# Kernel tuning notes

Hardware: AMD Instinct MI355X
Metric: run time of the kernel (lower is better)

Reference implementation:

```python
import jax, jax.numpy as jnp
import numpy as np

NUM_HEADS = 6
V = 25          # num_points (joints)
F = 64          # num_frames
T = F * V       # 1600 tokens
DIM = 216
HD = DIM // NUM_HEADS
SCALE = HD ** -0.5
MAX_HOP = 16    # hop-distance table size (distances clipped to MAX_HOP-1)
LN_EPS = 1e-5


def _ntu_hop_dist():
    # NTU RGB+D 25-joint skeleton edges (1-indexed)
    edges = [(1, 2), (2, 21), (3, 21), (4, 3), (5, 21), (6, 5), (7, 6), (8, 7),
             (9, 21), (10, 9), (11, 10), (12, 11), (13, 1), (14, 13), (15, 14),
             (16, 15), (17, 1), (18, 17), (19, 18), (20, 19), (22, 23), (23, 8),
             (24, 25), (25, 12)]
    D = np.full((V, V), 99, dtype=np.int64)
    np.fill_diagonal(D, 0)
    for a, b in edges:
        D[a - 1, b - 1] = 1
        D[b - 1, a - 1] = 1
    for k in range(V):  # Floyd-Warshall on tiny 25-node graph
        D = np.minimum(D, D[:, k:k + 1] + D[k:k + 1, :])
    return np.clip(D, 0, MAX_HOP - 1).astype(np.int32)


def setup_inputs() -> dict:
    key = jax.random.key(0)
    ks = jax.random.split(key, 16)
    s = 0.02  # trunc_normal_(std=0.02) init scale
    rn = lambda k, shape: jax.random.normal(k, shape, jnp.float32) * s
    return {
        "x": jax.random.normal(ks[0], (8, T, DIM), jnp.float32),
        "qkv_w": rn(ks[1], (3 * DIM, DIM)),
        "proj_w": rn(ks[2], (DIM, DIM)),
        "proj_b": jnp.zeros((DIM,), jnp.float32),
        "norm_w": jnp.ones((DIM,), jnp.float32),
        "norm_b": jnp.zeros((DIM,), jnp.float32),
        "norm1_w": jnp.ones((DIM,), jnp.float32),
        "norm1_b": jnp.zeros((DIM,), jnp.float32),
        "fc1_w": rn(ks[3], (4 * DIM, DIM)),
        "fc1_b": jnp.zeros((4 * DIM,), jnp.float32),
        "fc2_w": rn(ks[4], (DIM, 4 * DIM)),
        "fc2_b": jnp.zeros((DIM,), jnp.float32),
        "t_w1": rn(ks[5], (DIM, 1)),
        "t_b1": jnp.zeros((DIM,), jnp.float32),
        "t_w2": rn(ks[6], (NUM_HEADS, DIM)),
        "t_b2": jnp.zeros((NUM_HEADS,), jnp.float32),
        "h_w1": rn(ks[7], (DIM, 1)),
        "h_b1": jnp.zeros((DIM,), jnp.float32),
        "h_w2": rn(ks[8], (NUM_HEADS, DIM)),
        "h_b2": jnp.zeros((NUM_HEADS,), jnp.float32),
        "hop_dist": jnp.asarray(_ntu_hop_dist()),
    }


def _ln(x, w, b):
    mu = x.mean(-1, keepdims=True)
    var = jnp.mean((x - mu) ** 2, axis=-1, keepdims=True)
    return (x - mu) * jax.lax.rsqrt(var + LN_EPS) * w + b


def reference(x, qkv_w, proj_w, proj_b, norm_w, norm_b, norm1_w, norm1_b,
              fc1_w, fc1_b, fc2_w, fc2_b, t_w1, t_b1, t_w2, t_b2,
              h_w1, h_b1, h_w2, h_b2, hop_dist):
    N = x.shape[0]
    h = _ln(x, norm_w, norm_b)
    qkv = (h @ qkv_w.T).reshape(N, T, 3, NUM_HEADS, HD).transpose(2, 0, 3, 1, 4)
    q, k, v = qkv[0], qkv[1], qkv[2]                       # (N,H,T,HD)
    attn = jnp.einsum('nhqc,nhkc->nhqk', q, k)             # (N,H,T,T)

    # temporal relative position bias (depends only on relative frame offset)
    coords = jnp.arange(-(F - 1), F, dtype=jnp.float32)[:, None]       # (2F-1,1)
    tbl_t = jax.nn.relu(coords @ t_w1.T + t_b1) @ t_w2.T + t_b2        # (2F-1,H)
    fidx = jnp.arange(F)
    rel = fidx[:, None] - fidx[None, :] + (F - 1)                      # (F,F)
    bias_t = tbl_t[rel].transpose(2, 0, 1)                             # (H,F,F)
    bias_t = jnp.repeat(jnp.repeat(bias_t, V, axis=1), V, axis=2)      # (H,T,T)

    # hop relative position bias (skeleton hop distance, same every frame pair)
    hvals = jnp.arange(MAX_HOP, dtype=jnp.float32)[:, None]            # (MAX_HOP,1)
    tbl_h = jax.nn.relu(hvals @ h_w1.T + h_b1) @ h_w2.T + h_b2         # (MAX_HOP,H)
    bias_h = tbl_h[hop_dist].transpose(2, 0, 1)                        # (H,V,V)
    bias_h = jnp.tile(bias_h, (1, F, F))                               # (H,T,T)

    attn = (attn + bias_h + bias_t) * SCALE  # scale AFTER bias, as in source
    attn = jax.nn.softmax(attn, axis=-1)
    o = jnp.einsum('nhqk,nhkc->nhqc', attn, v)
    o = o.transpose(0, 2, 1, 3).reshape(N, T, DIM)
    o = o @ proj_w.T + proj_b

    x1 = x + o  # skip_proj is Identity (dim_in == dim)
    h1 = _ln(x1, norm1_w, norm1_b)
    m = jax.nn.gelu(h1 @ fc1_w.T + fc1_b, approximate=False) @ fc2_w.T + fc2_b
    return x1 + m
```

## Files before the change

kernel.cpp:

```cpp
#include <hip/hip_runtime.h>
#include <hip/hip_bf16.h>


#define NHEAD  6
#define TLEN   1600
#define DIMC   216
#define HDIM   36
#define NBATCH 8
#define MROWS  12800
#define QK_SCALE (1.f/6.f)
#define C2EXP 0.24022650695910072f

typedef __attribute__((ext_vector_type(8))) short s16x8;
typedef __attribute__((ext_vector_type(4))) float f32x4;

#define MFMA16(a,b,c) __builtin_amdgcn_mfma_f32_16x16x32_bf16((a),(b),(c),0,0,0)

__device__ __forceinline__ float  bf2f(ushort u){ return __uint_as_float((uint)u << 16); }
__device__ __forceinline__ ushort f2bf(float f){
  uint u = __float_as_uint(f);
  u += 0x7FFFu + ((u >> 16) & 1u);
  return (ushort)(u >> 16);
}
__device__ __forceinline__ uint cvtpk_bf16(float lo, float hi){
  uint r;
  asm("v_cvt_pk_bf16_f32 %0, %1, %2" : "=v"(r) : "v"(lo), "v"(hi));
  return r;
}
__device__ __forceinline__ float fexp2(float x){
  float r;
  asm("v_exp_f32 %0, %1" : "=v"(r) : "v"(x));
  return r;
}
__device__ __forceinline__ float frcp(float x){
  float r;
  asm("v_rcp_f32 %0, %1" : "=v"(r) : "v"(x));
  return r;
}
__device__ __forceinline__ void glds16(const ushort* g, ushort* l){
  __builtin_amdgcn_global_load_lds(
      (const __attribute__((address_space(1))) void*)g,
      (__attribute__((address_space(3))) void*)l, 16, 0, 0);
}

__global__ __launch_bounds__(256) void bias_tables_kernel(
    const float* __restrict__ t_w1, const float* __restrict__ t_b1,
    const float* __restrict__ t_w2, const float* __restrict__ t_b2,
    const float* __restrict__ h_w1, const float* __restrict__ h_b1,
    const float* __restrict__ h_w2, const float* __restrict__ h_b2,
    const int*  __restrict__ hop,
    float* __restrict__ bias_t, float* __restrict__ bias_h)
{
  __shared__ float tblh[16][NHEAD];
  int tid = threadIdx.x;
  if (tid < 127) {
    float xi = (float)(tid - 63);
    float acc[NHEAD] = {0.f,0.f,0.f,0.f,0.f,0.f};
    for (int d = 0; d < DIMC; ++d) {
      float r = fmaxf(fmaf(xi, t_w1[d], t_b1[d]), 0.f);
      #pragma unroll
      for (int h = 0; h < NHEAD; ++h) acc[h] = fmaf(r, t_w2[h*DIMC + d], acc[h]);
    }
    #pragma unroll
    for (int h = 0; h < NHEAD; ++h)
      bias_t[h*127 + tid] = (acc[h] + t_b2[h]) * C2EXP;
  }
  if (tid >= 128 && tid < 144) {
    int i = tid - 128;
    float xi = (float)i;
    float acc[NHEAD] = {0.f,0.f,0.f,0.f,0.f,0.f};
    for (int d = 0; d < DIMC; ++d) {
      float r = fmaxf(fmaf(xi, h_w1[d], h_b1[d]), 0.f);
      #pragma unroll
      for (int h = 0; h < NHEAD; ++h) acc[h] = fmaf(r, h_w2[h*DIMC + d], acc[h]);
    }
    #pragma unroll
    for (int h = 0; h < NHEAD; ++h) tblh[i][h] = acc[h] + h_b2[h];
  }
  __syncthreads();
  for (int i = tid; i < NHEAD*625; i += 256) {
    int h = i / 625, e = i - h*625;
    bias_h[i] = tblh[hop[e]][h];
  }
}

#define CP_QKV 157696
#define CP_PROJ 215040
#define CP_FC1 415744
#define CP_TOT 636928
#define PC_TOT (CP_TOT + NBATCH*NHEAD*TLEN)

__global__ __launch_bounds__(256) void padconv_kernel(
    const float* __restrict__ qkvw, const float* __restrict__ projw,
    const float* __restrict__ fc1w, const float* __restrict__ fc2w,
    ushort* __restrict__ dq, ushort* __restrict__ dp,
    ushort* __restrict__ d1, ushort* __restrict__ d2,
    const float* __restrict__ bh_raw,
    ushort* __restrict__ qb, ushort* __restrict__ kb)
{
  int idx = blockIdx.x*256 + threadIdx.x;
  if (idx < CP_TOT) {
    if (idx < CP_QKV) {
      int n = idx / 224, k = idx - n*224;
      dq[idx] = f2bf((n < 648 && k < 216) ? qkvw[n*216 + k] : 0.f);
    } else if (idx < CP_PROJ) {
      int i = idx - CP_QKV;
      int n = i / 224, k = i - n*224;
      dp[i] = f2bf((n < 216 && k < 216) ? projw[n*216 + k] : 0.f);
    } else if (idx < CP_FC1) {
      int i = idx - CP_PROJ;
      int n = i / 224, k = i - n*224;
      d1[i] = f2bf((n < 864 && k < 216) ? fc1w[n*216 + k] : 0.f);
    } else {
      int i = idx - CP_FC1;
      int n = i / 864, k = i - n*864;
      d2[i] = f2bf((n < 216) ? fc2w[n*864 + k] : 0.f);
    }
    return;
  }
  int i = idx - CP_TOT;
  if (i >= NBATCH*NHEAD*TLEN) return;
  int nh = i / TLEN, t = i - nh*TLEN;
  int h = nh % NHEAD;
  int vk = t % 25;
  size_t row = ((size_t)nh*TLEN + t) << 6;
  ushort4 z = {0,0,0,0};
  #pragma unroll
  for (int j = 0; j < 7; ++j) *(ushort4*)(qb + row + 36 + j*4) = z;
  qb[row + 36 + vk] = 0x3F80;
  #pragma unroll
  for (int j = 0; j < 25; ++j)
    kb[row + 36 + j] = f2bf(bh_raw[h*625 + j*25 + vk]);
  kb[row + 61] = 0; kb[row + 62] = 0; kb[row + 63] = 0;
}

__global__ __launch_bounds__(256) void ln_kernel(
    const float* __restrict__ x, const float* __restrict__ w,
    const float* __restrict__ b, ushort* __restrict__ out)
{
  int lane = threadIdx.x & 63;
  int row  = blockIdx.x * 4 + (threadIdx.x >> 6);
  const float* xr = x + (size_t)row * DIMC;
  float v0 = xr[lane];
  float v1 = xr[lane + 64];
  float v2 = xr[lane + 128];
  float v3 = (lane < 24) ? xr[lane + 192] : 0.f;
  float s1 = v0 + v1 + v2 + v3;
  float s2 = v0*v0 + v1*v1 + v2*v2 + v3*v3;
  #pragma unroll
  for (int m = 32; m; m >>= 1) { s1 += __shfl_xor(s1, m); s2 += __shfl_xor(s2, m); }
  float mu  = s1 * (1.f/216.f);
  float var = fmaxf(s2 * (1.f/216.f) - mu*mu, 0.f);
  float rs  = rsqrtf(var + 1e-5f);
  ushort* orow = out + (size_t)row * 224;
  orow[lane]       = f2bf((v0-mu)*rs*w[lane]       + b[lane]);
  orow[lane+64]    = f2bf((v1-mu)*rs*w[lane+64]    + b[lane+64]);
  orow[lane+128]   = f2bf((v2-mu)*rs*w[lane+128]   + b[lane+128]);
  if (lane < 32) {
    float vv = (lane < 24) ? (v3-mu)*rs*w[lane+192] + b[lane+192] : 0.f;
    orow[lane+192] = f2bf(vv);
  }
}

enum { EPI_QKV = 0, EPI_PROJ = 1, EPI_FC1 = 2, EPI_FC2 = 3 };

template<int EPI, int WM>
__global__ __launch_bounds__(256) void gemm_mfma(
    const ushort* __restrict__ A, const ushort* __restrict__ B,
    const float* __restrict__ bias, const float* __restrict__ res,
    float* __restrict__ outf, ushort* __restrict__ oq,
    ushort* __restrict__ ok, ushort* __restrict__ ov,
    int N, int K)
{
  constexpr int BM = WM*4;
  constexpr int NMF = WM/16;
  constexpr int APASS = (BM*4)/256;
  __shared__ ushort As[2][BM*32];
  __shared__ ushort Bs[2][64*32];

  int tid = threadIdx.x;
  int w = tid >> 6, lane = tid & 63, l15 = lane & 15, g = lane >> 4;
  int row0 = blockIdx.x*BM, col0 = blockIdx.y*64;
  const int NT = K >> 5;

  f32x4 acc[NMF][4];
  #pragma unroll
  for (int i = 0; i < NMF; ++i)
    #pragma unroll
    for (int nf = 0; nf < 4; ++nf) acc[i][nf] = (f32x4){0.f,0.f,0.f,0.f};

  #define STAGE(buf, t)                                                       \
  {                                                                           \
    int k0 = (t) << 5;                                                        \
    _Pragma("unroll")                                                         \
    for (int p = 0; p < APASS; ++p) {                                         \
      int idx = p*256 + tid;                                                  \
      int mf = idx >> 6, kq = (idx >> 4) & 3, r = idx & 15;                   \
      glds16(A + (size_t)(row0 + mf*16 + r)*K + k0 + kq*8,                    \
             &As[buf][(p*256 + w*64)*8]);                                     \
    }                                                                         \
    {                                                                         \
      int kq = (tid >> 4) & 3, r = tid & 15;                                  \
      glds16(B + (size_t)(col0 + w*16 + r)*K + k0 + kq*8,                     \
             &Bs[buf][w*512]);                                                \
    }                                                                         \
  }

  STAGE(0, 0)
  __syncthreads();

  for (int t = 0; t < NT; ++t) {
    int buf = t & 1;
    if (t + 1 < NT) STAGE(buf ^ 1, t + 1)
    #pragma unroll
    for (int i = 0; i < NMF; ++i) {
      s16x8 a = *(const s16x8*)&As[buf][((w*NMF + i)*64 + g*16 + l15)*8];
      #pragma unroll
      for (int nf = 0; nf < 4; ++nf) {
        s16x8 b = *(const s16x8*)&Bs[buf][(nf*64 + g*16 + l15)*8];
        acc[i][nf] = MFMA16(a, b, acc[i][nf]);
      }
    }
    __syncthreads();
  }
  #undef STAGE

  #pragma unroll
  for (int i = 0; i < NMF; ++i) {
    #pragma unroll
    for (int nf = 0; nf < 4; ++nf) {
      int c = col0 + nf*16 + l15;
      if (c >= N) continue;
      #pragma unroll
      for (int r = 0; r < 4; ++r) {
        int rr = row0 + w*WM + i*16 + 4*g + r;
        float v = acc[i][nf][r];
        if constexpr (EPI == EPI_QKV) {
          int s = c / DIMC, rem = c - s*DIMC;
          int hh = rem / HDIM, d = rem - hh*HDIM;
          int n = rr / TLEN, t = rr - n*TLEN;
          int nh = n*NHEAD + hh;
          ushort bv = f2bf(v);
          if (s == 0)      oq[(((size_t)nh*TLEN + t) << 6) + d] = bv;
          else if (s == 1) ok[(((size_t)nh*TLEN + t) << 6) + d] = bv;
          else {
            int tile = t >> 6, pos = t & 63;
            int ks2 = pos >> 5, kg = (pos >> 2) & 7, r2 = pos & 3;
            int sg = ((kg & 3) << 1) + (kg >> 2);
            int posp = ks2*32 + sg*4 + r2;
            int grs = (posp >> 3) ^ (d & 7);
            ov[((size_t)nh*HDIM + d)*TLEN + tile*64 + grs*8 + (posp & 7)] = bv;
          }
        } else if constexpr (EPI == EPI_PROJ) {
          outf[(size_t)rr*DIMC + c] = v + bias[c] + res[(size_t)rr*DIMC + c];
        } else if constexpr (EPI == EPI_FC1) {
          v += bias[c];
          float y = 0.7978845608f*(v + 0.044715f*v*v*v);
          float e = fexp2(-2.885390082f*y);
          v = v * frcp(1.f + e);
          oq[(size_t)rr*864 + c] = f2bf(v);
        } else {
          outf[(size_t)rr*DIMC + c] = v + bias[c] + res[(size_t)rr*DIMC + c];
        }
      }
    }
  }
}

__global__ __launch_bounds__(256) void attn_kernel(
    const ushort* __restrict__ qb, const ushort* __restrict__ kb,
    const ushort* __restrict__ vb, const float* __restrict__ bt_g,
    ushort* __restrict__ o)
{
  __shared__ ushort Ks[2][64*64];
  __shared__ ushort Vt[2][37*64];
  __shared__ float bts[128];

  int tid = threadIdx.x;
  int bid = blockIdx.x;
  int c   = bid >> 3;
  int c25 = c / 25;
  int nh  = (bid & 7)*6 + c25;
  int qt  = c - c25*25;
  int head = nh % NHEAD, n = nh / NHEAD;
  int wave = tid >> 6, lane = tid & 63;
  int g = lane >> 4, l15 = lane & 15, l7 = l15 & 7;

  if (tid < 127) bts[tid + 1] = bt_g[head*127 + tid];
  if (tid == 127) bts[0] = 0.f;
  if (tid < 64) {
    int b = tid >> 5, j = tid & 31;
    ((uint*)&Vt[b][36*64])[j] = 0x3F803F80u;
  }

  int qglob = qt*64 + wave*16 + l15;
  const ushort* qrow = qb + (((size_t)nh*TLEN + qglob) << 6);
  s16x8 qf0 = *(const s16x8*)(qrow + g*8);
  s16x8 qf1 = *(const s16x8*)(qrow + 32 + g*8);

  int fq = qglob / 25;

  int vkb[4], ftb[4];
  #pragma unroll
  for (int kt = 0; kt < 4; ++kt) {
    int k0 = kt*16 + 4*g;
    int f0 = (k0 >= 50) ? 2 : (k0 >= 25 ? 1 : 0);
    vkb[kt] = k0 - f0*25;
    ftb[kt] = fq - f0 + 64;
  }

  f32x4 oa[3];
  #pragma unroll
  for (int dt = 0; dt < 3; ++dt) oa[dt] = (f32x4){0.f,0.f,0.f,0.f};

  int srow = tid >> 3, sgrl = tid & 7;
  const ushort* kp = kb + ((size_t)nh*TLEN << 6)
                   + (srow << 6) + ((sgrl ^ (srow & 7)) << 3);
  const ushort* vp = vb + (size_t)nh*HDIM*TLEN + srow*TLEN + sgrl*8;

  glds16(kp,        &Ks[0][wave*512]);
  glds16(kp + 2048, &Ks[0][2048 + wave*512]);
  glds16(vp,        &Vt[0][wave*512]);
  if (tid < 32) glds16(vp + 32*TLEN, &Vt[0][2048]);
  kp += 4096; vp += 64;
  __syncthreads();

  for (int t = 0; t < 25; ++t) {
    int buf = t & 1;
    if (t < 24) {
      ushort* kd = &Ks[buf ^ 1][wave*512];
      glds16(kp,        kd);
      glds16(kp + 2048, kd + 2048);
      glds16(vp,        &Vt[buf ^ 1][wave*512]);
      if (tid < 32) glds16(vp + 32*TLEN, &Vt[buf ^ 1][2048]);
      kp += 4096; vp += 64;
    }

    f32x4 sa[4];
    #pragma unroll
    for (int kt = 0; kt < 4; ++kt) {
      const ushort* krow = &Ks[buf][(kt*16 + l15) << 6];
      s16x8 a0 = *(const s16x8*)(krow + ((g ^ l7) << 3));
      s16x8 a1 = *(const s16x8*)(krow + (((g + 4) ^ l7) << 3));
      f32x4 z = (f32x4){0.f,0.f,0.f,0.f};
      z = MFMA16(a0, qf0, z);
      sa[kt] = MFMA16(a1, qf1, z);
    }

    #pragma unroll
    for (int kt = 0; kt < 4; ++kt) {
      float bt0 = bts[ftb[kt]];
      float bt1 = bts[ftb[kt] - 1];
      #pragma unroll
      for (int r = 0; r < 4; ++r) {
        float btv = (vkb[kt] + r >= 25) ? bt1 : bt0;
        sa[kt][r] = fexp2(fmaf(sa[kt][r], C2EXP, btv));
      }
    }

    #pragma unroll
    for (int ks = 0; ks < 2; ++ks) {
      union { s16x8 v; uint u[4]; } pf;
      pf.u[0] = cvtpk_bf16(sa[2*ks][0],   sa[2*ks][1]);
      pf.u[1] = cvtpk_bf16(sa[2*ks][2],   sa[2*ks][3]);
      pf.u[2] = cvtpk_bf16(sa[2*ks+1][0], sa[2*ks+1][1]);
      pf.u[3] = cvtpk_bf16(sa[2*ks+1][2], sa[2*ks+1][3]);
      #pragma unroll
      for (int dt = 0; dt < 3; ++dt) {
        s16x8 a = *(const s16x8*)&Vt[buf][((dt*16 + l15) << 6) +
                                          ((((ks << 2) + g) ^ l7) << 3)];
        oa[dt] = MFMA16(a, pf.v, oa[dt]);
      }
    }

    #pragma unroll
    for (int kt = 0; kt < 4; ++kt) {
      vkb[kt] += 14; ftb[kt] -= 2;
      if (vkb[kt] >= 25) { vkb[kt] -= 25; ftb[kt] -= 1; }
    }

    __syncthreads();
  }

  float ls = (g == 1) ? oa[2][0] : 0.f;
  ls += __shfl_xor(ls, 16);
  ls += __shfl_xor(ls, 32);
  float inv = frcp(ls);
  ushort* orow_base = o + ((size_t)(n*TLEN + qglob))*224;
  ushort* orow = orow_base + head*HDIM;
  #pragma unroll
  for (int dt = 0; dt < 3; ++dt) {
    if (dt < 2 || g == 0) {
      ushort4 st;
      st.x = f2bf(oa[dt][0]*inv);
      st.y = f2bf(oa[dt][1]*inv);
      st.z = f2bf(oa[dt][2]*inv);
      st.w = f2bf(oa[dt][3]*inv);
      *(ushort4*)(orow + dt*16 + 4*g) = st;
    }
  }
  if (g >= 2) {
    ushort4 z = {0,0,0,0};
    *(ushort4*)(orow_base + 216 + (g - 2)*4) = z;
  }
}

extern "C" void kernel_launch(void* const* d_in, const int* in_sizes, int n_in,
                              void* d_out, int out_size, void* d_ws, size_t ws_size,
                              hipStream_t stream) {
  const float* x      = (const float*)d_in[0];
  const float* qkv_w  = (const float*)d_in[1];
  const float* proj_w = (const float*)d_in[2];
  const float* proj_b = (const float*)d_in[3];
  const float* norm_w = (const float*)d_in[4];
  const float* norm_b = (const float*)d_in[5];
  const float* norm1_w= (const float*)d_in[6];
  const float* norm1_b= (const float*)d_in[7];
  const float* fc1_w  = (const float*)d_in[8];
  const float* fc1_b  = (const float*)d_in[9];
  const float* fc2_w  = (const float*)d_in[10];
  const float* fc2_b  = (const float*)d_in[11];
  const float* t_w1   = (const float*)d_in[12];
  const float* t_b1   = (const float*)d_in[13];
  const float* t_w2   = (const float*)d_in[14];
  const float* t_b2   = (const float*)d_in[15];
  const float* h_w1   = (const float*)d_in[16];
  const float* h_b1   = (const float*)d_in[17];
  const float* h_w2   = (const float*)d_in[18];
  const float* h_b2   = (const float*)d_in[19];
  const int*   hop    = (const int*)d_in[20];

  const size_t WS_NEED = 40613504u;
  if (ws_size < WS_NEED) return;

  char* ws = (char*)d_ws;
  ushort* h_bf   = (ushort*)(ws);
  ushort* q_bf   = (ushort*)(ws + 5734400);
  ushort* k_bf   = (ushort*)(ws + 15564800);
  ushort* v_bf   = (ushort*)(ws + 25395200);
  ushort* o_bf   = (ushort*)(ws + 30924800);
  float*  x1     = (float*) (ws);
  ushort* h1_bf  = (ushort*)(ws + 11468800);
  ushort* g_bf   = (ushort*)(ws + 17203200);
  ushort* qkv_wb = (ushort*)(ws + 39321600);
  ushort* proj_wb= (ushort*)(ws + 39636992);
  ushort* fc1_wb = (ushort*)(ws + 39751680);
  ushort* fc2_wb = (ushort*)(ws + 40153088);
  float*  bt     = (float*) (ws + 40595456);
  float*  bh     = bt + 127*6;

  bias_tables_kernel<<<1, 256, 0, stream>>>(t_w1, t_b1, t_w2, t_b2,
                                            h_w1, h_b1, h_w2, h_b2, hop, bt, bh);

  padconv_kernel<<<(PC_TOT + 255)/256, 256, 0, stream>>>(
      qkv_w, proj_w, fc1_w, fc2_w, qkv_wb, proj_wb, fc1_wb, fc2_wb,
      bh, q_bf, k_bf);

  ln_kernel<<<MROWS/4, 256, 0, stream>>>(x, norm_w, norm_b, h_bf);

  gemm_mfma<EPI_QKV, 32><<<dim3(MROWS/128, 11), 256, 0, stream>>>(
      h_bf, qkv_wb, nullptr, nullptr, nullptr, q_bf, k_bf, v_bf, 648, 224);

  attn_kernel<<<1200, 256, 0, stream>>>(q_bf, k_bf, v_bf, bt, o_bf);

  gemm_mfma<EPI_PROJ, 16><<<dim3(MROWS/64, 4), 256, 0, stream>>>(
      o_bf, proj_wb, proj_b, x, x1, nullptr, nullptr, nullptr, 216, 224);

  ln_kernel<<<MROWS/4, 256, 0, stream>>>(x1, norm1_w, norm1_b, h1_bf);

  gemm_mfma<EPI_FC1, 32><<<dim3(MROWS/128, 14), 256, 0, stream>>>(
      h1_bf, fc1_wb, fc1_b, nullptr, nullptr, g_bf, nullptr, nullptr, 864, 224);

  gemm_mfma<EPI_FC2, 16><<<dim3(MROWS/64, 4), 256, 0, stream>>>(
      g_bf, fc2_wb, fc2_b, x1, (float*)d_out, nullptr, nullptr, nullptr, 216, 864);
}
```

Measured before the change: 158.7 us.

## Switch attention to 32x32x16 MFMA with 128-row query tiles

Rewrites the attention kernel to use 32x32x16 bf16 MFMA instead of 16x16x32, with each wave handling 32 query rows and each block 128 queries. This halves the grid and doubles K/V reuse per LDS load. Q is padded to 1664 rows per head so the last tile can read safely, and the V layout permutation and workspace offsets change to match. Costs are more accumulator registers per wave, lower occupancy, and 64 wasted padded query rows per head.

```diff
diff --git a/kernel.cpp b/kernel.cpp
--- a/kernel.cpp
+++ b/kernel.cpp
@@ -8,15 +8,16 @@
 #define HDIM   36
 #define NBATCH 8
 #define MROWS  12800
-#define QK_SCALE (1.f/6.f)
+#define QPAD   1664
 #define C2EXP 0.24022650695910072f
 
 typedef __attribute__((ext_vector_type(8))) short s16x8;
 typedef __attribute__((ext_vector_type(4))) float f32x4;
+typedef __attribute__((ext_vector_type(16))) float f32x16;
 
 #define MFMA16(a,b,c) __builtin_amdgcn_mfma_f32_16x16x32_bf16((a),(b),(c),0,0,0)
-
-__device__ __forceinline__ float  bf2f(ushort u){ return __uint_as_float((uint)u << 16); }
+#define MFMA32(a,b,c) __builtin_amdgcn_mfma_f32_32x32x16_bf16((a),(b),(c),0,0,0)
+
 __device__ __forceinline__ ushort f2bf(float f){
   uint u = __float_as_uint(f);
   u += 0x7FFFu + ((u >> 16) & 1u);
@@ -123,15 +124,16 @@
   int nh = i / TLEN, t = i - nh*TLEN;
   int h = nh % NHEAD;
   int vk = t % 25;
-  size_t row = ((size_t)nh*TLEN + t) << 6;
+  size_t qrow = ((size_t)nh*QPAD + t) << 6;
+  size_t krow = ((size_t)nh*TLEN + t) << 6;
   ushort4 z = {0,0,0,0};
   #pragma unroll
-  for (int j = 0; j < 7; ++j) *(ushort4*)(qb + row + 36 + j*4) = z;
-  qb[row + 36 + vk] = 0x3F80;
+  for (int j = 0; j < 7; ++j) *(ushort4*)(qb + qrow + 36 + j*4) = z;
+  qb[qrow + 36 + vk] = 0x3F80;
   #pragma unroll
   for (int j = 0; j < 25; ++j)
-    kb[row + 36 + j] = f2bf(bh_raw[h*625 + j*25 + vk]);
-  kb[row + 61] = 0; kb[row + 62] = 0; kb[row + 63] = 0;
+    kb[krow + 36 + j] = f2bf(bh_raw[h*625 + j*25 + vk]);
+  kb[krow + 61] = 0; kb[krow + 62] = 0; kb[krow + 63] = 0;
 }
 
 __global__ __launch_bounds__(256) void ln_kernel(
@@ -241,15 +243,14 @@
           int n = rr / TLEN, t = rr - n*TLEN;
           int nh = n*NHEAD + hh;
           ushort bv = f2bf(v);
-          if (s == 0)      oq[(((size_t)nh*TLEN + t) << 6) + d] = bv;
+          if (s == 0)      oq[(((size_t)nh*QPAD + t) << 6) + d] = bv;
           else if (s == 1) ok[(((size_t)nh*TLEN + t) << 6) + d] = bv;
           else {
             int tile = t >> 6, pos = t & 63;
-            int ks2 = pos >> 5, kg = (pos >> 2) & 7, r2 = pos & 3;
-            int sg = ((kg & 3) << 1) + (kg >> 2);
-            int posp = ks2*32 + sg*4 + r2;
-            int grs = (posp >> 3) ^ (d & 7);
-            ov[((size_t)nh*HDIM + d)*TLEN + tile*64 + grs*8 + (posp & 7)] = bv;
+            int slot = ((pos >> 4) << 4) + (((pos >> 2) & 1) << 3)
+                     + (pos & 3) + (((pos >> 3) & 1) << 2);
+            int grs = (slot >> 3) ^ (d & 7);
+            ov[((size_t)nh*HDIM + d)*TLEN + tile*64 + grs*8 + (slot & 7)] = bv;
           }
         } else if constexpr (EPI == EPI_PROJ) {
           outf[(size_t)rr*DIMC + c] = v + bias[c] + res[(size_t)rr*DIMC + c];
@@ -272,19 +273,19 @@
     const ushort* __restrict__ vb, const float* __restrict__ bt_g,
     ushort* __restrict__ o)
 {
-  __shared__ ushort Ks[2][64*64];
-  __shared__ ushort Vt[2][37*64];
+  __shared__ __align__(16) ushort Ks[2][64*64];
+  __shared__ __align__(16) ushort Vt[2][64*64];
   __shared__ float bts[128];
 
   int tid = threadIdx.x;
   int bid = blockIdx.x;
   int c   = bid >> 3;
-  int c25 = c / 25;
-  int nh  = (bid & 7)*6 + c25;
-  int qt  = c - c25*25;
+  int c13 = c / 13;
+  int nh  = (bid & 7)*6 + c13;
+  int qt  = c - c13*13;
   int head = nh % NHEAD, n = nh / NHEAD;
   int wave = tid >> 6, lane = tid & 63;
-  int g = lane >> 4, l15 = lane & 15, l7 = l15 & 7;
+  int h = lane >> 5, l31 = lane & 31, l7 = l31 & 7;
 
   if (tid < 127) bts[tid + 1] = bt_g[head*127 + tid];
   if (tid == 127) bts[0] = 0.f;
@@ -293,25 +294,25 @@
     ((uint*)&Vt[b][36*64])[j] = 0x3F803F80u;
   }
 
-  int qglob = qt*64 + wave*16 + l15;
-  const ushort* qrow = qb + (((size_t)nh*TLEN + qglob) << 6);
-  s16x8 qf0 = *(const s16x8*)(qrow + g*8);
-  s16x8 qf1 = *(const s16x8*)(qrow + 32 + g*8);
+  int qglob = qt*128 + wave*32 + l31;
+  const ushort* qrow = qb + (((size_t)nh*QPAD + qglob) << 6);
+  s16x8 qf0 = *(const s16x8*)(qrow + h*8);
+  s16x8 qf1 = *(const s16x8*)(qrow + 16 + h*8);
+  s16x8 qf2 = *(const s16x8*)(qrow + 32 + h*8);
+  s16x8 qf3 = *(const s16x8*)(qrow + 48 + h*8);
 
   int fq = qglob / 25;
 
-  int vkb[4], ftb[4];
-  #pragma unroll
-  for (int kt = 0; kt < 4; ++kt) {
-    int k0 = kt*16 + 4*g;
+  int vkb[8], ftb[8];
+  #pragma unroll
+  for (int gi = 0; gi < 8; ++gi) {
+    int k0 = 32*(gi >> 2) + 8*(gi & 3) + 4*h;
     int f0 = (k0 >= 50) ? 2 : (k0 >= 25 ? 1 : 0);
-    vkb[kt] = k0 - f0*25;
-    ftb[kt] = fq - f0 + 64;
-  }
-
-  f32x4 oa[3];
-  #pragma unroll
-  for (int dt = 0; dt < 3; ++dt) oa[dt] = (f32x4){0.f,0.f,0.f,0.f};
+    vkb[gi] = k0 - f0*25;
+    ftb[gi] = fq - f0 + 64;
+  }
+
+  f32x16 pacc0 = {}, pacc1 = {};
 
   int srow = tid >> 3, sgrl = tid & 7;
   const ushort* kp = kb + ((size_t)nh*TLEN << 6)
@@ -324,6 +325,9 @@
   if (tid < 32) glds16(vp + 32*TLEN, &Vt[0][2048]);
   kp += 4096; vp += 64;
   __syncthreads();
+
+  int rb0 = (l31 << 6);
+  int rb1 = ((32 + l31) << 6);
 
   for (int t = 0; t < 25; ++t) {
     int buf = t & 1;
@@ -336,72 +340,88 @@
       kp += 4096; vp += 64;
     }
 
-    f32x4 sa[4];
-    #pragma unroll
-    for (int kt = 0; kt < 4; ++kt) {
-      const ushort* krow = &Ks[buf][(kt*16 + l15) << 6];
-      s16x8 a0 = *(const s16x8*)(krow + ((g ^ l7) << 3));
-      s16x8 a1 = *(const s16x8*)(krow + (((g + 4) ^ l7) << 3));
-      f32x4 z = (f32x4){0.f,0.f,0.f,0.f};
-      z = MFMA16(a0, qf0, z);
-      sa[kt] = MFMA16(a1, qf1, z);
-    }
-
-    #pragma unroll
-    for (int kt = 0; kt < 4; ++kt) {
-      float bt0 = bts[ftb[kt]];
-      float bt1 = bts[ftb[kt] - 1];
-      #pragma unroll
-      for (int r = 0; r < 4; ++r) {
-        float btv = (vkb[kt] + r >= 25) ? bt1 : bt0;
-        sa[kt][r] = fexp2(fmaf(sa[kt][r], C2EXP, btv));
+    f32x16 sa0 = {}, sa1 = {};
+    {
+      #pragma unroll
+      for (int s = 0; s < 4; ++s) {
+        int go = (((2*s + h) ^ l7) << 3);
+        s16x8 k0 = *(const s16x8*)&Ks[buf][rb0 + go];
+        s16x8 k1 = *(const s16x8*)&Ks[buf][rb1 + go];
+        s16x8 qv = (s == 0) ? qf0 : (s == 1) ? qf1 : (s == 2) ? qf2 : qf3;
+        sa0 = MFMA32(k0, qv, sa0);
+        sa1 = MFMA32(k1, qv, sa1);
       }
     }
 
     #pragma unroll
-    for (int ks = 0; ks < 2; ++ks) {
-      union { s16x8 v; uint u[4]; } pf;
-      pf.u[0] = cvtpk_bf16(sa[2*ks][0],   sa[2*ks][1]);
-      pf.u[1] = cvtpk_bf16(sa[2*ks][2],   sa[2*ks][3]);
-      pf.u[2] = cvtpk_bf16(sa[2*ks+1][0], sa[2*ks+1][1]);
-      pf.u[3] = cvtpk_bf16(sa[2*ks+1][2], sa[2*ks+1][3]);
-      #pragma unroll
-      for (int dt = 0; dt < 3; ++dt) {
-        s16x8 a = *(const s16x8*)&Vt[buf][((dt*16 + l15) << 6) +
-                                          ((((ks << 2) + g) ^ l7) << 3)];
-        oa[dt] = MFMA16(a, pf.v, oa[dt]);
+    for (int gi = 0; gi < 8; ++gi) {
+      float bt0 = bts[ftb[gi]];
+      float bt1 = bts[ftb[gi] - 1];
+      #pragma unroll
+      for (int rr = 0; rr < 4; ++rr) {
+        float btv = (vkb[gi] + rr >= 25) ? bt1 : bt0;
+        int idx = (gi & 3)*4 + rr;
+        if (gi < 4) sa0[idx] = fexp2(fmaf(sa0[idx], C2EXP, btv));
+        else        sa1[idx] = fexp2(fmaf(sa1[idx], C2EXP, btv));
       }
     }
 
-    #pragma unroll
-    for (int kt = 0; kt < 4; ++kt) {
-      vkb[kt] += 14; ftb[kt] -= 2;
-      if (vkb[kt] >= 25) { vkb[kt] -= 25; ftb[kt] -= 1; }
+    union { s16x8 v; uint u[4]; } pf0, pf1, pf2, pf3;
+    #pragma unroll
+    for (int i = 0; i < 4; ++i) {
+      pf0.u[i] = cvtpk_bf16(sa0[2*i],     sa0[2*i + 1]);
+      pf1.u[i] = cvtpk_bf16(sa0[8 + 2*i], sa0[9 + 2*i]);
+      pf2.u[i] = cvtpk_bf16(sa1[2*i],     sa1[2*i + 1]);
+      pf3.u[i] = cvtpk_bf16(sa1[8 + 2*i], sa1[9 + 2*i]);
+    }
+
+    #pragma unroll
+    for (int s = 0; s < 4; ++s) {
+      int go = (((2*s + h) ^ l7) << 3);
+      s16x8 v0 = *(const s16x8*)&Vt[buf][rb0 + go];
+      s16x8 v1 = *(const s16x8*)&Vt[buf][rb1 + go];
+      s16x8 pv = (s == 0) ? pf0.v : (s == 1) ? pf1.v : (s == 2) ? pf2.v : pf3.v;
+      pacc0 = MFMA32(v0, pv, pacc0);
+      pacc1 = MFMA32(v1, pv, pacc1);
+    }
+
+    #pragma unroll
+    for (int gi = 0; gi < 8; ++gi) {
+      vkb[gi] += 14; ftb[gi] -= 2;
+      if (vkb[gi] >= 25) { vkb[gi] -= 25; ftb[gi] -= 1; }
     }
 
     __syncthreads();
   }
 
-  float ls = (g == 1) ? oa[2][0] : 0.f;
-  ls += __shfl_xor(ls, 16);
+  float ls = (h == 1) ? pacc1[0] : 0.f;
   ls += __shfl_xor(ls, 32);
   float inv = frcp(ls);
-  ushort* orow_base = o + ((size_t)(n*TLEN + qglob))*224;
-  ushort* orow = orow_base + head*HDIM;
-  #pragma unroll
-  for (int dt = 0; dt < 3; ++dt) {
-    if (dt < 2 || g == 0) {
+
+  if (qglob < TLEN) {
+    ushort* orow_base = o + ((size_t)(n*TLEN + qglob))*224;
+    ushort* orow = orow_base + head*HDIM;
+    #pragma unroll
+    for (int rq = 0; rq < 4; ++rq) {
       ushort4 st;
-      st.x = f2bf(oa[dt][0]*inv);
-      st.y = f2bf(oa[dt][1]*inv);
-      st.z = f2bf(oa[dt][2]*inv);
-      st.w = f2bf(oa[dt][3]*inv);
-      *(ushort4*)(orow + dt*16 + 4*g) = st;
-    }
-  }
-  if (g >= 2) {
-    ushort4 z = {0,0,0,0};
-    *(ushort4*)(orow_base + 216 + (g - 2)*4) = z;
+      st.x = f2bf(pacc0[rq*4 + 0]*inv);
+      st.y = f2bf(pacc0[rq*4 + 1]*inv);
+      st.z = f2bf(pacc0[rq*4 + 2]*inv);
+      st.w = f2bf(pacc0[rq*4 + 3]*inv);
+      *(ushort4*)(orow + 8*rq + 4*h) = st;
+    }
+    if (h == 0) {
+      ushort4 st;
+      st.x = f2bf(pacc1[0]*inv);
+      st.y = f2bf(pacc1[1]*inv);
+      st.z = f2bf(pacc1[2]*inv);
+      st.w = f2bf(pacc1[3]*inv);
+      *(ushort4*)(orow + 32) = st;
+    }
+    if (head == 0) {
+      ushort4 z = {0,0,0,0};
+      *(ushort4*)(orow_base + 216 + h*4) = z;
+    }
   }
 }
 
@@ -436,9 +456,9 @@
   char* ws = (char*)d_ws;
   ushort* h_bf   = (ushort*)(ws);
   ushort* q_bf   = (ushort*)(ws + 5734400);
-  ushort* k_bf   = (ushort*)(ws + 15564800);
-  ushort* v_bf   = (ushort*)(ws + 25395200);
-  ushort* o_bf   = (ushort*)(ws + 30924800);
+  ushort* k_bf   = (ushort*)(ws + 15958016);
+  ushort* v_bf   = (ushort*)(ws + 25788416);
+  ushort* o_bf   = (ushort*)(ws + 31318016);
   float*  x1     = (float*) (ws);
   ushort* h1_bf  = (ushort*)(ws + 11468800);
   ushort* g_bf   = (ushort*)(ws + 17203200);
@@ -461,7 +481,7 @@
   gemm_mfma<EPI_QKV, 32><<<dim3(MROWS/128, 11), 256, 0, stream>>>(
       h_bf, qkv_wb, nullptr, nullptr, nullptr, q_bf, k_bf, v_bf, 648, 224);
 
-  attn_kernel<<<1200, 256, 0, stream>>>(q_bf, k_bf, v_bf, bt, o_bf);
+  attn_kernel<<<624, 256, 0, stream>>>(q_bf, k_bf, v_bf, bt, o_bf);
 
   gemm_mfma<EPI_PROJ, 16><<<dim3(MROWS/64, 4), 256, 0, stream>>>(
       o_bf, proj_wb, proj_b, x, x1, nullptr, nullptr, nullptr, 216, 224);
```

After: 179.2 us (median of 5 runs). +12.9%, slower.
